# Optimization experiments

Hardware: AMD Instinct MI355X
Metric: run time of the kernel (lower is better)

The kernel has to match this reference:

```python
import jax, jax.numpy as jnp
import numpy as np

N_HEAD = 12

def setup_inputs() -> dict:
    key = jax.random.key(0)
    k1, k2, k3 = jax.random.split(key, 3)
    B, T, C = 4, 2048, 768
    x = jax.random.normal(k1, (B, T, C), dtype=jnp.float32)
    # c_attn params (Linear(n_embd, 3*n_embd)); stored as [in, out] for x @ W
    W_attn = jax.random.normal(k2, (C, 3 * C), dtype=jnp.float32) * (1.0 / np.sqrt(C))
    b_attn = jax.random.normal(k3, (3 * C,), dtype=jnp.float32) * 0.02
    return {"x": x, "W_attn": W_attn, "b_attn": b_attn}

def reference(x, W_attn, b_attn):
    B, T, C = x.shape
    H = N_HEAD
    Dh = C // H
    qkv = x @ W_attn + b_attn                      # [B,T,3C]
    q, k, v = jnp.split(qkv, 3, axis=-1)
    q = q.reshape(B, T, H, Dh)
    k = k.reshape(B, T, H, Dh)
    v = v.reshape(B, T, H, Dh)
    scale = 1.0 / np.sqrt(Dh)
    # scaled QK^T per head: [B,H,T,T]
    scores = jnp.einsum('bqhd,bkhd->bhqk', q * scale, k)
    causal = jnp.tril(jnp.ones((T, T), dtype=bool))  # [T,T]
    # masked-to--inf then ReLU == zero out non-causal and clamp at 0
    p = jnp.where(causal, jnp.maximum(scores, 0.0), 0.0)
    y = jnp.einsum('bhqk,bkhd->bqhd', p, v).reshape(B, T, C)
    return y
```

## Files before the change

kernel.cpp:

```cpp
#include <hip/hip_runtime.h>
#include <cstdint>
#include <cstddef>

typedef unsigned short u16;
typedef unsigned int u32;
typedef __bf16 bf16x8 __attribute__((ext_vector_type(8)));
typedef float f32x4 __attribute__((ext_vector_type(4)));

__device__ __forceinline__ u16 f2bf(float f) {
    unsigned int x = __builtin_bit_cast(unsigned int, f);
    x += 0x7FFFu + ((x >> 16) & 1u);
    return (u16)(x >> 16);
}

__device__ __forceinline__ bf16x8 ldfrag(const u16* p) {
    bf16x8 r;
    __builtin_memcpy(&r, (const u16*)__builtin_assume_aligned(p, 16), 16);
    return r;
}

__device__ __forceinline__ int4 ldg16(const u16* p) {
    int4 r;
    __builtin_memcpy(&r, (const u16*)__builtin_assume_aligned(p, 16), 16);
    return r;
}

__device__ __forceinline__ void async16(u16* lds, const u16* g) {
    __builtin_amdgcn_global_load_lds(
        (const __attribute__((address_space(1))) void*)g,
        (__attribute__((address_space(3))) void*)lds,
        16, 0, 0);
}

__global__ __launch_bounds__(256) void cvt_bf16(const float* __restrict__ in,
                                                u16* __restrict__ out, int n) {
    int i = (blockIdx.x * 256 + threadIdx.x) * 4;
    if (i >= n) return;
    float4 v = *reinterpret_cast<const float4*>(in + i);
    union { u16 e[4]; unsigned long long u; } w;
    w.e[0] = f2bf(v.x); w.e[1] = f2bf(v.y); w.e[2] = f2bf(v.z); w.e[3] = f2bf(v.w);
    *reinterpret_cast<unsigned long long*>(out + i) = w.u;
}

__global__ __launch_bounds__(256) void wt_transpose(const float* __restrict__ W,
                                                    u16* __restrict__ Wt) {
    const int R = 768, Ccols = 2304;
    __shared__ float tile[32][33];
    const int bx = blockIdx.x * 32;
    const int by = blockIdx.y * 32;
    const int tx = threadIdx.x & 31, ty = threadIdx.x >> 5;
    #pragma unroll
    for (int i = 0; i < 32; i += 8)
        tile[ty + i][tx] = W[(size_t)(by + ty + i) * Ccols + bx + tx];
    __syncthreads();
    #pragma unroll
    for (int i = 0; i < 32; i += 8)
        Wt[(size_t)(bx + ty + i) * R + by + tx] = f2bf(tile[tx][ty + i]);
}

__global__ __launch_bounds__(256) void qkv_gemm(const u16* __restrict__ A,
                                                const u16* __restrict__ Bt,
                                                const float* __restrict__ bias,
                                                u16* __restrict__ C) {
    const int N = 2304, K = 768;
    __shared__ __align__(16) u16 sA[128 * 64];
    __shared__ __align__(16) u16 sB[128 * 64];
    const int t = threadIdx.x;
    const int wave = t >> 6, lane = t & 63;
    const int quad = lane >> 4, l16 = lane & 15;
    const int wr = wave >> 1, wc = wave & 1;
    const int m0 = blockIdx.y * 128, n0 = blockIdx.x * 128;

    const int srow_base = wave * 8 + (lane >> 3);
    const int schunk = lane & 7;
    const int swz = (lane >> 3) & 7;

    f32x4 acc[4][4] = {};

    for (int k0 = 0; k0 < K; k0 += 64) {
        __syncthreads();
        #pragma unroll
        for (int j = 0; j < 4; ++j) {
            const int row = j * 32 + srow_base;
            const int dch = schunk ^ swz;
            async16(sA + j * 2048 + wave * 512, A + (size_t)(m0 + row) * K + k0 + dch * 8);
            async16(sB + j * 2048 + wave * 512, Bt + (size_t)(n0 + row) * K + k0 + dch * 8);
        }
        __syncthreads();

        bf16x8 af[4][2], bfr[4][2];
        const int rsw = l16 & 7;
        #pragma unroll
        for (int i = 0; i < 4; ++i)
            #pragma unroll
            for (int h = 0; h < 2; ++h) {
                af[i][h] = ldfrag(sA + (wr * 64 + i * 16 + l16) * 64 + (((h * 4 + quad) ^ rsw) << 3));
                bfr[i][h] = ldfrag(sB + (wc * 64 + i * 16 + l16) * 64 + (((h * 4 + quad) ^ rsw) << 3));
            }
        #pragma unroll
        for (int h = 0; h < 2; ++h)
            #pragma unroll
            for (int i = 0; i < 4; ++i)
                #pragma unroll
                for (int j = 0; j < 4; ++j)
                    acc[i][j] = __builtin_amdgcn_mfma_f32_16x16x32_bf16(af[i][h], bfr[j][h], acc[i][j], 0, 0, 0);
    }

    #pragma unroll
    for (int i = 0; i < 4; ++i)
        #pragma unroll
        for (int j = 0; j < 4; ++j) {
            const int col = n0 + wc * 64 + j * 16 + l16;
            const float bc = bias[col];
            const float scale = (col < 768) ? 0.125f : 1.0f;
            #pragma unroll
            for (int r = 0; r < 4; ++r) {
                const int row = m0 + wr * 64 + i * 16 + quad * 4 + r;
                C[(size_t)row * N + col] = f2bf((acc[i][j][r] + bc) * scale);
            }
        }
}

__global__ __launch_bounds__(256, 3) void attn_kernel(const u16* __restrict__ qkv,
                                                      float* __restrict__ out) {
    const int T = 2048, C3 = 2304, Cc = 768, Dh = 64;

    const int bid = blockIdx.x;
    const int rr = bid >> 8;
    const int ss = bid & 255;
    const int x = ss & 15;
    const int qa = (rr == 0) ? x : (rr == 1) ? (15 - x) : ((x + 8) & 15);
    const int qb = 31 - qa;
    const int hb = (ss >> 4) + (rr << 4);
    const int h = hb % 12, b = hb / 12;

    const int t = threadIdx.x;
    const int wave = t >> 6, lane = t & 63;
    const int quad = lane >> 4, l16 = lane & 15;

    __shared__ __align__(16) u16 sK[2][64 * 64];
    __shared__ __align__(16) u32 sVt[2][64 * 36];
    __shared__ __align__(16) u16 sP[128 * 72];

    const u16* qbase = qkv + (size_t)b * T * C3 + (size_t)h * Dh;
    const u16* kbase = qbase + Cc;
    const u16* vbase = qbase + 2 * Cc;

    bf16x8 qf[8][2];
    #pragma unroll
    for (int cg = 0; cg < 8; ++cg) {
        const int qrow = ((cg < 4) ? qa * 64 : (qb * 64 - 64)) + cg * 16 + l16;
        const u16* p = qbase + (size_t)qrow * C3 + quad * 8;
        qf[cg][0] = ldfrag(p);
        qf[cg][1] = ldfrag(p + 32);
    }

    f32x4 oacc[2][4] = {};

    const int tp = t & 31, dg = t >> 5;
    const int krow_b = wave * 8 + (lane >> 3);
    const int kswz = (lane >> 3) & 7;
    const int kch = (lane & 7) ^ kswz;

    int4 v0r, v1r;
    auto loadV = [&](int it) {
        const u16* vp = vbase + (size_t)(it * 64 + 2 * tp) * C3 + dg * 8;
        v0r = ldg16(vp);
        v1r = ldg16(vp + C3);
    };
    auto stageK = [&](int it, int bi) {
        #pragma unroll
        for (int j = 0; j < 2; ++j)
            async16(&sK[bi][0] + j * 2048 + wave * 512,
                    kbase + (size_t)(it * 64 + j * 32 + krow_b) * C3 + kch * 8);
    };
    auto writeV = [&](int bi) {
        union { int4 v; u16 e[8]; } ua, ub;
        ua.v = v0r; ub.v = v1r;
        #pragma unroll
        for (int i = 0; i < 8; ++i)
            sVt[bi][(dg * 8 + i) * 36 + tp] = (u32)ua.e[i] | ((u32)ub.e[i] << 16);
    };

    loadV(0);
    stageK(0, 0);
    writeV(0);
    __syncthreads();

    int buf = 0;
    for (int it = 0; it <= qb; ++it) {
        const bool more = (it < qb);
        if (more) { loadV(it + 1); stageK(it + 1, buf ^ 1); }

        const bool act_a = (it <= qa);

        bf16x8 kf0, kf1;
        {
            const u16* kr = &sK[buf][0] + (wave * 16 + l16) * 64;
            const int rsw = l16 & 7;
            kf0 = ldfrag(kr + ((quad ^ rsw) << 3));
            kf1 = ldfrag(kr + (((quad + 4) ^ rsw) << 3));
        }
        const int cg_lo = act_a ? 0 : 4;
        #pragma unroll
        for (int cg = 7; cg >= 0; --cg) {
            if (cg < cg_lo) break;
            f32x4 s = {};
            s = __builtin_amdgcn_mfma_f32_16x16x32_bf16(kf0, qf[cg][0], s, 0, 0, 0);
            s = __builtin_amdgcn_mfma_f32_16x16x32_bf16(kf1, qf[cg][1], s, 0, 0, 0);
            const bool diag = (cg < 4) ? (it == qa) : (it == qb);
            u32 bits[4];
            #pragma unroll
            for (int r = 0; r < 4; ++r) {
                float v = fmaxf(s[r], 0.0f);
                if (diag && (wave * 16 + quad * 4 + r > (cg & 3) * 16 + l16)) v = 0.0f;
                bits[r] = __builtin_bit_cast(u32, v);
            }
            u32 pk[2];
            pk[0] = (bits[1] & 0xFFFF0000u) | (bits[0] >> 16);
            pk[1] = (bits[3] & 0xFFFF0000u) | (bits[2] >> 16);
            __builtin_memcpy((u16*)__builtin_assume_aligned(
                                 sP + (cg * 16 + l16) * 72 + wave * 16 + quad * 4, 8),
                             pk, 8);
        }
        __syncthreads();

        const u16* sVb = (const u16*)sVt[buf];
        #pragma unroll
        for (int kk = 0; kk < 2; ++kk) {
            bf16x8 ap1 = ldfrag(sP + (64 + wave * 16 + l16) * 72 + kk * 32 + quad * 8);
            bf16x8 ap0;
            if (act_a) ap0 = ldfrag(sP + (wave * 16 + l16) * 72 + kk * 32 + quad * 8);
            #pragma unroll
            for (int dt = 0; dt < 4; ++dt) {
                bf16x8 bv = ldfrag(sVb + (dt * 16 + l16) * 72 + kk * 32 + quad * 8);
                oacc[1][dt] = __builtin_amdgcn_mfma_f32_16x16x32_bf16(ap1, bv, oacc[1][dt], 0, 0, 0);
                if (act_a)
                    oacc[0][dt] = __builtin_amdgcn_mfma_f32_16x16x32_bf16(ap0, bv, oacc[0][dt], 0, 0, 0);
            }
        }

        if (more) writeV(buf ^ 1);
        __syncthreads();
        buf ^= 1;
    }

    #pragma unroll
    for (int g = 0; g < 2; ++g)
        #pragma unroll
        for (int dt = 0; dt < 4; ++dt)
            #pragma unroll
            for (int r = 0; r < 4; ++r) {
                const int tok = (g == 0 ? qa * 64 : qb * 64) + wave * 16 + quad * 4 + r;
                const int c = h * Dh + dt * 16 + l16;
                out[((size_t)b * T + tok) * Cc + c] = oacc[g][dt][r];
            }
}

extern "C" void kernel_launch(void* const* d_in, const int* in_sizes, int n_in,
                              void* d_out, int out_size, void* d_ws, size_t ws_size,
                              hipStream_t stream) {
    const float* x    = (const float*)d_in[0];
    const float* W    = (const float*)d_in[1];
    const float* bias = (const float*)d_in[2];
    float* out = (float*)d_out;

    char* ws = (char*)d_ws;
    const size_t xb_bytes = (size_t)8192 * 768 * 2;
    const size_t wt_bytes = (size_t)2304 * 768 * 2;
    u16* xb  = (u16*)ws;
    u16* Wt  = (u16*)(ws + xb_bytes);
    u16* qkv = (u16*)(ws + xb_bytes + wt_bytes);

    cvt_bf16<<<6144, 256, 0, stream>>>(x, xb, 8192 * 768);
    wt_transpose<<<dim3(72, 24), 256, 0, stream>>>(W, Wt);
    qkv_gemm<<<dim3(18, 64), 256, 0, stream>>>(xb, Wt, bias, qkv);
    attn_kernel<<<768, 256, 0, stream>>>(qkv, out);
}
```

Baseline: 186.9 us.

## Emit transposed V from GEMM, async-stage V in attention, double-buffer GEMM

```diff
diff --git a/kernel.cpp b/kernel.cpp
--- a/kernel.cpp
+++ b/kernel.cpp
@@ -4,6 +4,7 @@
 
 typedef unsigned short u16;
 typedef unsigned int u32;
+typedef unsigned long long u64;
 typedef __bf16 bf16x8 __attribute__((ext_vector_type(8)));
 typedef float f32x4 __attribute__((ext_vector_type(4)));
 
@@ -15,12 +16,6 @@
 
 __device__ __forceinline__ bf16x8 ldfrag(const u16* p) {
     bf16x8 r;
-    __builtin_memcpy(&r, (const u16*)__builtin_assume_aligned(p, 16), 16);
-    return r;
-}
-
-__device__ __forceinline__ int4 ldg16(const u16* p) {
-    int4 r;
     __builtin_memcpy(&r, (const u16*)__builtin_assume_aligned(p, 16), 16);
     return r;
 }
@@ -32,98 +27,125 @@
         16, 0, 0);
 }
 
-__global__ __launch_bounds__(256) void cvt_bf16(const float* __restrict__ in,
-                                                u16* __restrict__ out, int n) {
-    int i = (blockIdx.x * 256 + threadIdx.x) * 4;
-    if (i >= n) return;
-    float4 v = *reinterpret_cast<const float4*>(in + i);
-    union { u16 e[4]; unsigned long long u; } w;
-    w.e[0] = f2bf(v.x); w.e[1] = f2bf(v.y); w.e[2] = f2bf(v.z); w.e[3] = f2bf(v.w);
-    *reinterpret_cast<unsigned long long*>(out + i) = w.u;
-}
-
-__global__ __launch_bounds__(256) void wt_transpose(const float* __restrict__ W,
-                                                    u16* __restrict__ Wt) {
-    const int R = 768, Ccols = 2304;
-    __shared__ float tile[32][33];
-    const int bx = blockIdx.x * 32;
-    const int by = blockIdx.y * 32;
-    const int tx = threadIdx.x & 31, ty = threadIdx.x >> 5;
-    #pragma unroll
-    for (int i = 0; i < 32; i += 8)
-        tile[ty + i][tx] = W[(size_t)(by + ty + i) * Ccols + bx + tx];
-    __syncthreads();
-    #pragma unroll
-    for (int i = 0; i < 32; i += 8)
-        Wt[(size_t)(bx + ty + i) * R + by + tx] = f2bf(tile[tx][ty + i]);
+__global__ __launch_bounds__(256) void prep(const float* __restrict__ x,
+                                            u16* __restrict__ xb,
+                                            const float* __restrict__ W,
+                                            u16* __restrict__ Wt) {
+    const int bx = blockIdx.x;
+    if (bx < 6144) {
+        const int i = (bx * 256 + threadIdx.x) * 4;
+        float4 v = *reinterpret_cast<const float4*>(x + i);
+        union { u16 e[4]; u64 u; } w;
+        w.e[0] = f2bf(v.x); w.e[1] = f2bf(v.y); w.e[2] = f2bf(v.z); w.e[3] = f2bf(v.w);
+        *reinterpret_cast<u64*>(xb + i) = w.u;
+    } else {
+        const int R = 768, Ccols = 2304;
+        __shared__ float tile[32][33];
+        const int bb = bx - 6144;
+        const int bxc = (bb % 72) * 32;
+        const int byr = (bb / 72) * 32;
+        const int tx = threadIdx.x & 31, ty = threadIdx.x >> 5;
+        #pragma unroll
+        for (int i = 0; i < 32; i += 8)
+            tile[ty + i][tx] = W[(size_t)(byr + ty + i) * Ccols + bxc + tx];
+        __syncthreads();
+        #pragma unroll
+        for (int i = 0; i < 32; i += 8)
+            Wt[(size_t)(bxc + ty + i) * R + byr + tx] = f2bf(tile[tx][ty + i]);
+    }
 }
 
 __global__ __launch_bounds__(256) void qkv_gemm(const u16* __restrict__ A,
                                                 const u16* __restrict__ Bt,
                                                 const float* __restrict__ bias,
-                                                u16* __restrict__ C) {
-    const int N = 2304, K = 768;
-    __shared__ __align__(16) u16 sA[128 * 64];
-    __shared__ __align__(16) u16 sB[128 * 64];
+                                                u16* __restrict__ qk,
+                                                u16* __restrict__ Vt) {
+    const int N = 2304, K = 768, QKW = 1536;
+    __shared__ __align__(16) u16 sA[2][128 * 32];
+    __shared__ __align__(16) u16 sB[2][128 * 32];
     const int t = threadIdx.x;
     const int wave = t >> 6, lane = t & 63;
     const int quad = lane >> 4, l16 = lane & 15;
     const int wr = wave >> 1, wc = wave & 1;
     const int m0 = blockIdx.y * 128, n0 = blockIdx.x * 128;
 
-    const int srow_base = wave * 8 + (lane >> 3);
-    const int schunk = lane & 7;
-    const int swz = (lane >> 3) & 7;
+    const int srow = wave * 32 + (lane >> 2);
+    const int sseg = lane & 3;
 
     f32x4 acc[4][4] = {};
 
-    for (int k0 = 0; k0 < K; k0 += 64) {
-        __syncthreads();
-        #pragma unroll
-        for (int j = 0; j < 4; ++j) {
-            const int row = j * 32 + srow_base;
-            const int dch = schunk ^ swz;
-            async16(sA + j * 2048 + wave * 512, A + (size_t)(m0 + row) * K + k0 + dch * 8);
-            async16(sB + j * 2048 + wave * 512, Bt + (size_t)(n0 + row) * K + k0 + dch * 8);
-        }
-        __syncthreads();
-
-        bf16x8 af[4][2], bfr[4][2];
-        const int rsw = l16 & 7;
+    auto stage = [&](int k0, int bi) {
+        #pragma unroll
+        for (int j = 0; j < 2; ++j) {
+            const int row = srow + j * 16;
+            async16(&sA[bi][0] + wave * 1024 + j * 512,
+                    A + (size_t)(m0 + row) * K + k0 + sseg * 8);
+            async16(&sB[bi][0] + wave * 1024 + j * 512,
+                    Bt + (size_t)(n0 + row) * K + k0 + sseg * 8);
+        }
+    };
+
+    stage(0, 0);
+    __syncthreads();
+
+    int buf = 0;
+    for (int k0 = 0; k0 < K; k0 += 32) {
+        if (k0 + 32 < K) stage(k0 + 32, buf ^ 1);
+
+        bf16x8 af[4], bfr[4];
         #pragma unroll
         for (int i = 0; i < 4; ++i)
-            #pragma unroll
-            for (int h = 0; h < 2; ++h) {
-                af[i][h] = ldfrag(sA + (wr * 64 + i * 16 + l16) * 64 + (((h * 4 + quad) ^ rsw) << 3));
-                bfr[i][h] = ldfrag(sB + (wc * 64 + i * 16 + l16) * 64 + (((h * 4 + quad) ^ rsw) << 3));
-            }
-        #pragma unroll
-        for (int h = 0; h < 2; ++h)
-            #pragma unroll
-            for (int i = 0; i < 4; ++i)
+            af[i] = ldfrag(&sA[buf][0] + (wr * 64 + i * 16 + l16) * 32 + quad * 8);
+        #pragma unroll
+        for (int j = 0; j < 4; ++j)
+            bfr[j] = ldfrag(&sB[buf][0] + (wc * 64 + j * 16 + l16) * 32 + quad * 8);
+        #pragma unroll
+        for (int i = 0; i < 4; ++i)
+            #pragma unroll
+            for (int j = 0; j < 4; ++j)
+                acc[i][j] = __builtin_amdgcn_mfma_f32_16x16x32_bf16(af[i], bfr[j], acc[i][j], 0, 0, 0);
+
+        __syncthreads();
+        buf ^= 1;
+    }
+
+    if (n0 < 1536) {
+        #pragma unroll
+        for (int i = 0; i < 4; ++i)
+            #pragma unroll
+            for (int j = 0; j < 4; ++j) {
+                const int col = n0 + wc * 64 + j * 16 + l16;
+                const float bc = bias[col];
+                const float scale = (col < 768) ? 0.125f : 1.0f;
                 #pragma unroll
-                for (int j = 0; j < 4; ++j)
-                    acc[i][j] = __builtin_amdgcn_mfma_f32_16x16x32_bf16(af[i][h], bfr[j][h], acc[i][j], 0, 0, 0);
-    }
-
-    #pragma unroll
-    for (int i = 0; i < 4; ++i)
-        #pragma unroll
-        for (int j = 0; j < 4; ++j) {
-            const int col = n0 + wc * 64 + j * 16 + l16;
-            const float bc = bias[col];
-            const float scale = (col < 768) ? 0.125f : 1.0f;
-            #pragma unroll
-            for (int r = 0; r < 4; ++r) {
-                const int row = m0 + wr * 64 + i * 16 + quad * 4 + r;
-                C[(size_t)row * N + col] = f2bf((acc[i][j][r] + bc) * scale);
-            }
-        }
-}
-
-__global__ __launch_bounds__(256, 3) void attn_kernel(const u16* __restrict__ qkv,
+                for (int r = 0; r < 4; ++r) {
+                    const int row = m0 + wr * 64 + i * 16 + quad * 4 + r;
+                    qk[(size_t)row * QKW + col] = f2bf((acc[i][j][r] + bc) * scale);
+                }
+            }
+    } else {
+        const int h = ((n0 - 1536) >> 6) + wc;
+        #pragma unroll
+        for (int i = 0; i < 4; ++i) {
+            const int grow = m0 + wr * 64 + i * 16 + quad * 4;
+            const int b = grow >> 11, tok = grow & 2047;
+            #pragma unroll
+            for (int j = 0; j < 4; ++j) {
+                const int d = j * 16 + l16;
+                const float bc = bias[1536 + h * 64 + d];
+                u32 lo = (u32)f2bf(acc[i][j][0] + bc) | ((u32)f2bf(acc[i][j][1] + bc) << 16);
+                u32 hi = (u32)f2bf(acc[i][j][2] + bc) | ((u32)f2bf(acc[i][j][3] + bc) << 16);
+                u64 pk = (u64)lo | ((u64)hi << 32);
+                *reinterpret_cast<u64*>(Vt + ((size_t)((b * 12 + h) * 64 + d)) * 2048 + tok) = pk;
+            }
+        }
+    }
+}
+
+__global__ __launch_bounds__(256, 3) void attn_kernel(const u16* __restrict__ qk,
+                                                      const u16* __restrict__ Vt,
                                                       float* __restrict__ out) {
-    const int T = 2048, C3 = 2304, Cc = 768, Dh = 64;
+    const int T = 2048, QKW = 1536, Cc = 768, Dh = 64;
 
     const int bid = blockIdx.x;
     const int rr = bid >> 8;
@@ -139,58 +161,48 @@
     const int quad = lane >> 4, l16 = lane & 15;
 
     __shared__ __align__(16) u16 sK[2][64 * 64];
-    __shared__ __align__(16) u32 sVt[2][64 * 36];
+    __shared__ __align__(16) u16 sV[2][64 * 64];
     __shared__ __align__(16) u16 sP[128 * 72];
 
-    const u16* qbase = qkv + (size_t)b * T * C3 + (size_t)h * Dh;
-    const u16* kbase = qbase + Cc;
-    const u16* vbase = qbase + 2 * Cc;
+    const u16* qbase = qk + (size_t)b * T * QKW + (size_t)h * Dh;
+    const u16* kbase = qbase + 768;
+    const u16* vtb = Vt + (size_t)(b * 12 + h) * 64 * 2048;
 
     bf16x8 qf[8][2];
     #pragma unroll
     for (int cg = 0; cg < 8; ++cg) {
         const int qrow = ((cg < 4) ? qa * 64 : (qb * 64 - 64)) + cg * 16 + l16;
-        const u16* p = qbase + (size_t)qrow * C3 + quad * 8;
+        const u16* p = qbase + (size_t)qrow * QKW + quad * 8;
         qf[cg][0] = ldfrag(p);
         qf[cg][1] = ldfrag(p + 32);
     }
 
     f32x4 oacc[2][4] = {};
 
-    const int tp = t & 31, dg = t >> 5;
-    const int krow_b = wave * 8 + (lane >> 3);
-    const int kswz = (lane >> 3) & 7;
-    const int kch = (lane & 7) ^ kswz;
-
-    int4 v0r, v1r;
-    auto loadV = [&](int it) {
-        const u16* vp = vbase + (size_t)(it * 64 + 2 * tp) * C3 + dg * 8;
-        v0r = ldg16(vp);
-        v1r = ldg16(vp + C3);
-    };
+    const int srow = wave * 8 + (lane >> 3);
+    const int sch = (lane & 7) ^ ((lane >> 3) & 7);
+
     auto stageK = [&](int it, int bi) {
         #pragma unroll
         for (int j = 0; j < 2; ++j)
             async16(&sK[bi][0] + j * 2048 + wave * 512,
-                    kbase + (size_t)(it * 64 + j * 32 + krow_b) * C3 + kch * 8);
+                    kbase + (size_t)(it * 64 + j * 32 + srow) * QKW + sch * 8);
     };
-    auto writeV = [&](int bi) {
-        union { int4 v; u16 e[8]; } ua, ub;
-        ua.v = v0r; ub.v = v1r;
-        #pragma unroll
-        for (int i = 0; i < 8; ++i)
-            sVt[bi][(dg * 8 + i) * 36 + tp] = (u32)ua.e[i] | ((u32)ub.e[i] << 16);
+    auto stageV = [&](int it, int bi) {
+        #pragma unroll
+        for (int j = 0; j < 2; ++j)
+            async16(&sV[bi][0] + j * 2048 + wave * 512,
+                    vtb + (size_t)(j * 32 + srow) * 2048 + it * 64 + sch * 8);
     };
 
-    loadV(0);
     stageK(0, 0);
-    writeV(0);
+    stageV(0, 0);
     __syncthreads();
 
     int buf = 0;
     for (int it = 0; it <= qb; ++it) {
         const bool more = (it < qb);
-        if (more) { loadV(it + 1); stageK(it + 1, buf ^ 1); }
+        if (more) stageK(it + 1, buf ^ 1);
 
         const bool act_a = (it <= qa);
 
@@ -225,7 +237,8 @@
         }
         __syncthreads();
 
-        const u16* sVb = (const u16*)sVt[buf];
+        if (more) stageV(it + 1, buf ^ 1);
+
         #pragma unroll
         for (int kk = 0; kk < 2; ++kk) {
             bf16x8 ap1 = ldfrag(sP + (64 + wave * 16 + l16) * 72 + kk * 32 + quad * 8);
@@ -233,14 +246,14 @@
             if (act_a) ap0 = ldfrag(sP + (wave * 16 + l16) * 72 + kk * 32 + quad * 8);
             #pragma unroll
             for (int dt = 0; dt < 4; ++dt) {
-                bf16x8 bv = ldfrag(sVb + (dt * 16 + l16) * 72 + kk * 32 + quad * 8);
+                const int d = dt * 16 + l16;
+                bf16x8 bv = ldfrag(&sV[buf][0] + d * 64 + (((kk * 4 + quad) ^ (l16 & 7)) << 3));
                 oacc[1][dt] = __builtin_amdgcn_mfma_f32_16x16x32_bf16(ap1, bv, oacc[1][dt], 0, 0, 0);
                 if (act_a)
                     oacc[0][dt] = __builtin_amdgcn_mfma_f32_16x16x32_bf16(ap0, bv, oacc[0][dt], 0, 0, 0);
             }
         }
 
-        if (more) writeV(buf ^ 1);
         __syncthreads();
         buf ^= 1;
     }
@@ -268,12 +281,13 @@
     char* ws = (char*)d_ws;
     const size_t xb_bytes = (size_t)8192 * 768 * 2;
     const size_t wt_bytes = (size_t)2304 * 768 * 2;
-    u16* xb  = (u16*)ws;
-    u16* Wt  = (u16*)(ws + xb_bytes);
-    u16* qkv = (u16*)(ws + xb_bytes + wt_bytes);
-
-    cvt_bf16<<<6144, 256, 0, stream>>>(x, xb, 8192 * 768);
-    wt_transpose<<<dim3(72, 24), 256, 0, stream>>>(W, Wt);
-    qkv_gemm<<<dim3(18, 64), 256, 0, stream>>>(xb, Wt, bias, qkv);
-    attn_kernel<<<768, 256, 0, stream>>>(qkv, out);
-}
+    const size_t qk_bytes = (size_t)8192 * 1536 * 2;
+    u16* xb = (u16*)ws;
+    u16* Wt = (u16*)(ws + xb_bytes);
+    u16* qk = (u16*)(ws + xb_bytes + wt_bytes);
+    u16* Vt = (u16*)(ws + xb_bytes + wt_bytes + qk_bytes);
+
+    prep<<<6144 + 1728, 256, 0, stream>>>(x, xb, W, Wt);
+    qkv_gemm<<<dim3(18, 64), 256, 0, stream>>>(xb, Wt, bias, qk, Vt);
+    attn_kernel<<<768, 256, 0, stream>>>(qk, Vt, out);
+}
```

After: 199.6 us. 1.07x slower.
